# Performance work log

Hardware: AMD Instinct MI355X
Metric: run time of the kernel (lower is better)

The kernel has to match this reference:

```python
import jax, jax.numpy as jnp
import numpy as np

H = 768    # bert hidden size
P = 64     # num dialogue pairs
L = 2 * P  # interleaved (user,system) sequence length
C = 2      # num_classes (CRF tags)
LAM = 0.1  # lambda_mle


def setup_inputs():
    key = jax.random.key(0)
    ks = jax.random.split(key, 21)
    def rn(k, shape, s=0.05):
        return jax.random.normal(k, shape, dtype=jnp.float32) * s
    G = 4 * H
    return {
        "user_repr": rn(ks[0], (P, H), 1.0),
        "system_repr": rn(ks[1], (P, H), 1.0),
        "post_Wih0": rn(ks[2], (2, G, H)), "post_Whh0": rn(ks[3], (2, G, H)), "post_b0": rn(ks[4], (2, G)),
        "post_Wih1": rn(ks[5], (2, G, 2 * H)), "post_Whh1": rn(ks[6], (2, G, H)), "post_b1": rn(ks[7], (2, G)),
        "prior_Wih0": rn(ks[8], (2, G, H)), "prior_Whh0": rn(ks[9], (2, G, H)), "prior_b0": rn(ks[10], (2, G)),
        "prior_Wih1": rn(ks[11], (2, G, 2 * H)), "prior_Whh1": rn(ks[12], (2, G, H)), "prior_b1": rn(ks[13], (2, G)),
        "post_proj_W": rn(ks[14], (C, 2 * H)), "post_proj_b": rn(ks[15], (C,)),
        "prior_proj_W": rn(ks[16], (C, 2 * H)), "prior_proj_b": rn(ks[17], (C,)),
        "transitions": rn(ks[18], (C, C), 0.1),
        "user_I_label": jax.random.randint(ks[19], (1, P), 0, C),
        "system_I_label": jax.random.randint(ks[20], (1, P), 0, C),
    }


def _lstm_dir(x, mask, Wih, Whh, b, reverse):
    # x: [P, L, Din]; mask: [P, L] bool (True = valid step). Masked steps freeze state,
    # so each row computes the LSTM over its own prefix exactly as the per-pair loop does.
    Pn, Ln, _ = x.shape
    Hn = Whh.shape[1]
    xw = jnp.einsum('pld,gd->plg', x, Wih) + b  # [P, L, 4H] input projections (torch gate order i,f,g,o)
    def step(carry, inp):
        h, c = carry
        xw_t, m_t = inp
        gates = xw_t + h @ Whh.T
        i, f, g, o = jnp.split(gates, 4, axis=-1)
        c2 = jax.nn.sigmoid(f) * c + jax.nn.sigmoid(i) * jnp.tanh(g)
        h2 = jax.nn.sigmoid(o) * jnp.tanh(c2)
        m = m_t[:, None]
        h = jnp.where(m, h2, h)
        c = jnp.where(m, c2, c)
        return (h, c), h
    init = (jnp.zeros((Pn, Hn), x.dtype), jnp.zeros((Pn, Hn), x.dtype))
    _, hs = jax.lax.scan(step, init, (jnp.swapaxes(xw, 0, 1), mask.T), reverse=reverse)
    return jnp.swapaxes(hs, 0, 1)  # [P, L, H]


def _bilstm(x, mask, layers):
    for Wih, Whh, b in layers:
        fwd = _lstm_dir(x, mask, Wih[0], Whh[0], b[0], False)
        bwd = _lstm_dir(x, mask, Wih[1], Whh[1], b[1], True)
        x = jnp.concatenate([fwd, bwd], axis=-1)
    return x


def _forward(user_repr, system_repr,
             post_Wih0, post_Whh0, post_b0, post_Wih1, post_Whh1, post_b1,
             prior_Wih0, prior_Whh0, prior_b0, prior_Wih1, prior_Whh1, prior_b1,
             post_proj_W, post_proj_b, prior_proj_W, prior_proj_b, transitions, labs):
    seq = jnp.stack([user_repr, system_repr], axis=1).reshape(L, H)  # interleaved u0,s0,u1,s1,...
    l = 2 * (jnp.arange(P) + 1)                 # prefix length per pair
    t = jnp.arange(L)
    mask = t[None, :] < l[:, None]              # [P, L]
    xb = jnp.broadcast_to(seq[None], (P, L, H))
    # posterior branch: biLSTM over each prefix, then emissions
    post_out = _bilstm(xb, mask, [(post_Wih0, post_Whh0, post_b0), (post_Wih1, post_Whh1, post_b1)])
    em = post_out @ post_proj_W.T + post_proj_b  # [P, L, C]
    mf = mask.astype(em.dtype)
    # CRF gold score per pair
    e_lab = jnp.take_along_axis(em, jnp.broadcast_to(labs[None, :, None], (P, L, 1)), axis=2)[..., 0]
    trans_step = transitions[labs[:-1], labs[1:]]  # [L-1]
    gold = (e_lab * mf).sum(1) + (trans_step[None, :] * mf[:, 1:]).sum(1)
    # CRF forward algorithm (log partition), masked scan over time
    def fstep(alpha, inp):
        em_t, m_t = inp  # [P, C], [P]
        new = jax.nn.logsumexp(alpha[:, :, None] + transitions[None, :, :] + em_t[:, None, :], axis=1)
        return jnp.where(m_t[:, None], new, alpha), None
    alpha, _ = jax.lax.scan(fstep, em[:, 0, :], (jnp.swapaxes(em[:, 1:, :], 0, 1), mask[:, 1:].T))
    total = jax.nn.logsumexp(alpha, axis=1)
    loss_crf = jnp.mean(total - gold)
    # prior branch: prefix minus last token, take last valid hidden
    mask_p = t[None, :] < (l - 1)[:, None]
    prior_out = _bilstm(xb, mask_p, [(prior_Wih0, prior_Whh0, prior_b0), (prior_Wih1, prior_Whh1, prior_b1)])
    prior_last = jnp.take_along_axis(prior_out, jnp.broadcast_to((l - 2)[:, None, None], (P, 1, 2 * H)), axis=1)[:, 0, :]
    prior_emis = prior_last @ prior_proj_W.T + prior_proj_b  # [P, C]
    post_last = jnp.take_along_axis(em, jnp.broadcast_to((l - 1)[:, None, None], (P, 1, C)), axis=1)[:, 0, :]
    loss_mle = jnp.mean((prior_emis - jax.lax.stop_gradient(post_last)) ** 2)
    return loss_crf, loss_mle, loss_crf + LAM * loss_mle


def reference(user_repr, system_repr,
              post_Wih0, post_Whh0, post_b0, post_Wih1, post_Whh1, post_b1,
              prior_Wih0, prior_Whh0, prior_b0, prior_Wih1, prior_Whh1, prior_b1,
              post_proj_W, post_proj_b, prior_proj_W, prior_proj_b, transitions,
              user_I_label, system_I_label):
    labs = jnp.stack([user_I_label[0], system_I_label[0]], axis=1).reshape(L)
    return _forward(user_repr, system_repr,
                    post_Wih0, post_Whh0, post_b0, post_Wih1, post_Whh1, post_b1,
                    prior_Wih0, prior_Whh0, prior_b0, prior_Wih1, prior_Whh1, prior_b1,
                    post_proj_W, post_proj_b, prior_proj_W, prior_proj_b, transitions, labs)
```

## Files before the change

### kernel.cpp

```cpp
#include <hip/hip_runtime.h>


typedef short v8s __attribute__((ext_vector_type(8)));
typedef float v4f __attribute__((ext_vector_type(4)));
typedef unsigned short u16;

#define MFMA(a, b, c) __builtin_amdgcn_mfma_f32_16x16x32_bf16((a), (b), (c), 0, 0, 0)

static constexpr size_t WMAT    = (size_t)96 * 3072 * 8;
static constexpr size_t SLOT16  = (size_t)96 * 16 * 8;
static constexpr size_t SLOT64  = (size_t)96 * 64 * 8;
static constexpr size_t SLOT128 = (size_t)96 * 128 * 8;

static constexpr size_t OFF_EM   = 0;
static constexpr size_t SZ_EM    = (size_t)2 * 64 * 128 * 2 * 4;
static constexpr size_t OFF_XW0  = OFF_EM + SZ_EM;
static constexpr size_t SZ_XW    = (size_t)4 * 128 * 3072 * 4;
static constexpr size_t OFF_XW1  = OFF_XW0 + SZ_XW;
static constexpr size_t OFF_SEQ  = OFF_XW1 + SZ_XW;
static constexpr size_t SZ_SEQ   = SLOT128 * 2;
static constexpr size_t OFF_LABS = OFF_SEQ + SZ_SEQ;
static constexpr size_t OFF_BAR  = OFF_LABS + 512;
static constexpr size_t SZ_BAR   = 16384;
static constexpr size_t OFF_W0   = OFF_BAR + SZ_BAR;
static constexpr size_t SZ_W4    = (size_t)4 * WMAT * 2;
static constexpr size_t OFF_W1X  = OFF_W0 + SZ_W4;
static constexpr size_t OFF_W1R  = OFF_W1X + SZ_W4;
static constexpr size_t OFF_F0   = OFF_W1R + SZ_W4;
static constexpr size_t SZ_F0    = (size_t)2 * 129 * SLOT16 * 2;
static constexpr size_t OFF_H0F  = OFF_F0 + SZ_F0;
static constexpr size_t SZ_H0F   = (size_t)2 * SLOT128 * 2;
static constexpr size_t OFF_B0   = OFF_H0F + SZ_H0F;
static constexpr size_t SZ_S64   = (size_t)2 * 129 * SLOT64 * 2;
static constexpr size_t OFF_F1   = OFF_B0 + SZ_S64;
static constexpr size_t OFF_B1   = OFF_F1 + SZ_S64;
static constexpr size_t WS_NEED  = OFF_B1 + SZ_S64;

static __device__ __forceinline__ u16 f2b(float f) {
  unsigned int u = __float_as_uint(f);
  unsigned int r = (u + 0x7FFFu + ((u >> 16) & 1u)) >> 16;
  return (u16)r;
}
static __device__ __forceinline__ float b2f(u16 u) {
  return __uint_as_float(((unsigned int)u) << 16);
}
static __device__ __forceinline__ float sigf(float x) {
  return 1.0f / (1.0f + __expf(-x));
}
static __device__ __forceinline__ float tanhfast(float x) {
  return 1.0f - 2.0f / (__expf(2.0f * x) + 1.0f);
}
static __device__ __forceinline__ float lse2(float a, float b) {
  float mx = fmaxf(a, b);
  return mx + __logf(__expf(a - mx) + __expf(b - mx));
}

static __device__ __forceinline__ void gl2lds16(const void* g, void* l) {
  __builtin_amdgcn_global_load_lds((const __attribute__((address_space(1))) unsigned int*)g,
                                   (__attribute__((address_space(3))) unsigned int*)l,
                                   16, 0, 0);
}

static __device__ __forceinline__ void tree_bar(unsigned* base, int grp, unsigned target) {
  if (threadIdx.x == 0) {
    asm volatile("s_waitcnt vmcnt(0)" ::: "memory");
    asm volatile("buffer_wbl2 sc1" ::: "memory");
    asm volatile("s_waitcnt vmcnt(0)" ::: "memory");
    unsigned o1 = __hip_atomic_fetch_add(base + grp * 32, 1u,
                                         __ATOMIC_RELAXED, __HIP_MEMORY_SCOPE_AGENT);
    if ((o1 % 6u) == 5u) {
      unsigned o2 = __hip_atomic_fetch_add(base + 256, 1u,
                                           __ATOMIC_RELAXED, __HIP_MEMORY_SCOPE_AGENT);
      if ((o2 % 8u) == 7u) {
        __hip_atomic_fetch_add(base + 288, 1u,
                               __ATOMIC_RELAXED, __HIP_MEMORY_SCOPE_AGENT);
      }
    }
    int guard = 0;
    while (__hip_atomic_load(base + 288, __ATOMIC_RELAXED,
                             __HIP_MEMORY_SCOPE_AGENT) < target) {
      __builtin_amdgcn_s_sleep(4);
      if (++guard > (1 << 20)) break;
    }
    asm volatile("buffer_inv sc0 sc1" ::: "memory");
    asm volatile("s_waitcnt vmcnt(0)" ::: "memory");
  }
  __syncthreads();
}

__global__ void init_zero(u16* f0a, u16* f0b, u16* b0a, u16* b0b,
                          u16* f1a, u16* f1b, u16* b1a, u16* b1b, unsigned* bars) {
  int idx = blockIdx.x * 256 + threadIdx.x;
  if (idx < (int)SLOT16) { f0a[idx] = 0; f0b[idx] = 0; }
  b0a[idx] = 0; b0b[idx] = 0;
  f1a[idx] = 0; f1b[idx] = 0;
  b1a[idx] = 0; b1b[idx] = 0;
  if (idx < 4096) bars[idx] = 0;
}

__global__ void build_seq(const float* user, const float* sysr, const int* ulab,
                          const int* slab, u16* seqkp, int* labs) {
  int idx = blockIdx.x * 256 + threadIdx.x;
  int t = idx / 768;
  int hh = idx - t * 768;
  float v = (t & 1) ? sysr[(t >> 1) * 768 + hh] : user[(t >> 1) * 768 + hh];
  seqkp[((size_t)(hh >> 3) * 128 + t) * 8 + (hh & 7)] = f2b(v);
  if (idx < 128) labs[idx] = (idx & 1) ? slab[idx >> 1] : ulab[idx >> 1];
}

__global__ void cvt_w(const float* postWhh0, const float* priWhh0,
                      const float* postWih1, const float* priWih1,
                      const float* postWhh1, const float* priWhh1,
                      u16* W0kp, u16* W1xkp, u16* W1rkp) {
  int mat = blockIdx.y;
  int grp = mat >> 2;
  int sub = mat & 3;
  int mm = sub >> 1;
  int dirw = sub & 1;
  const float* src;
  int stride, coff;
  u16* dstb;
  if (grp == 0)      { src = mm ? priWhh0 : postWhh0; stride = 768;  coff = 0;   dstb = W0kp; }
  else if (grp == 1) { src = mm ? priWih1 : postWih1; stride = 1536; coff = 768; dstb = W1xkp; }
  else               { src = mm ? priWhh1 : postWhh1; stride = 768;  coff = 0;   dstb = W1rkp; }
  src += (size_t)dirw * 3072 * stride;
  int cid = blockIdx.x * 256 + threadIdx.x;
  int g = cid / 96;
  int kb = cid - g * 96;
  int gate = g / 768;
  int unit = g - gate * 768;
  int gp = unit * 4 + gate;
  const float* s = src + (size_t)g * stride + coff + (size_t)kb * 8;
  union { u16 h[8]; int4 v; } u;
#pragma unroll
  for (int j = 0; j < 8; ++j) u.h[j] = f2b(s[j]);
  ((int4*)(dstb + (size_t)sub * WMAT))[(size_t)kb * 3072 + gp] = u.v;
}

__global__ void __launch_bounds__(256) xw_gemm(const u16* Akp, unsigned long long Astride,
                                               const float* Wm0, const float* Wm1, int wstride,
                                               const float* bm0, const float* bm1, float* out) {
  __shared__ u16 lds[48 * 64 * 8];
  int tid = threadIdx.x;
  int lane = tid & 63;
  int wave = tid >> 6;
  int md = blockIdx.y;
  int m = md >> 1;
  int dir = md & 1;
  const u16* A = Akp + (size_t)m * Astride;
  const float* W = (m ? Wm1 : Wm0) + (size_t)dir * 3072 * wstride;
  const float* b = (m ? bm1 : bm0) + dir * 3072;
  int g0 = blockIdx.x * 64;
  int quad = lane >> 4, l15 = lane & 15;
  v4f acc[2][4];
#pragma unroll
  for (int a = 0; a < 2; ++a)
#pragma unroll
    for (int nt = 0; nt < 4; ++nt) acc[a][nt] = (v4f){0.f, 0.f, 0.f, 0.f};

  for (int hfl = 0; hfl < 2; ++hfl) {
    if (hfl) __syncthreads();
    for (int it = 0; it < 12; ++it) {
      int ck = it * 256 + tid;
      int kb = ck >> 6;
      int r = ck & 63;
      int g = g0 + r;
      const float* s = W + (size_t)g * wstride + (size_t)(hfl * 48 + kb) * 8;
      union { u16 h[8]; int4 v; } u;
#pragma unroll
      for (int j = 0; j < 8; ++j) u.h[j] = f2b(s[j]);
      *(int4*)(lds + (size_t)ck * 8) = u.v;
    }
    __syncthreads();
    for (int lt = 0; lt < 12; ++lt) {
      int kblk = (hfl * 12 + lt) * 4 + quad;
      v8s a0 = ((const v8s*)A)[(size_t)kblk * 128 + (wave * 2 + 0) * 16 + l15];
      v8s a1 = ((const v8s*)A)[(size_t)kblk * 128 + (wave * 2 + 1) * 16 + l15];
#pragma unroll
      for (int nt = 0; nt < 4; ++nt) {
        v8s bb = *(const v8s*)(lds + ((size_t)((lt * 4 + quad) * 64) + nt * 16 + l15) * 8);
        acc[0][nt] = MFMA(a0, bb, acc[0][nt]);
        acc[1][nt] = MFMA(a1, bb, acc[1][nt]);
      }
    }
  }
#pragma unroll
  for (int a = 0; a < 2; ++a)
#pragma unroll
    for (int nt = 0; nt < 4; ++nt) {
      int g = g0 + nt * 16 + l15;
      float bv = b[g];
#pragma unroll
      for (int r = 0; r < 4; ++r) {
        int trow = (wave * 2 + a) * 16 + quad * 4 + r;
        out[(size_t)(md * 128 + trow) * 3072 + g] = acc[a][nt][r] + bv;
      }
    }
}

__global__ void __launch_bounds__(256, 1) phase1_k(const u16* W0kp, const float* xw0,
                                                   u16* B0, u16* F0, u16* h0f,
                                                   unsigned* bars) {
  extern __shared__ u16 ldsraw[];
  v8s* lw = (v8s*)ldsraw;
  const int tid = threadIdx.x;
  const int w = tid >> 6, lane = tid & 63, l15 = lane & 15, l4 = lane >> 4;
  const int b = blockIdx.x;
  const int chain = (b & 7) >> 1;
  const int ci = ((b >> 3) << 1) | (b & 1);
  const int grp = ci / 6;
  const int jb = ci << 4;
  const int m = chain & 1;
  const bool isf = chain >= 2;
  const int mat = m * 2 + (isf ? 0 : 1);
  unsigned* bbase = bars + chain * 512;

  {
    const v8s* Ws = (const v8s*)(W0kp) + (size_t)mat * (WMAT / 8);
    const size_t rowb = (size_t)jb * 4;
    for (int i = 0; i < 24; ++i) {
      int idx = i * 256 + tid;
      int kg = idx >> 6, r = idx & 63;
      gl2lds16(Ws + (size_t)kg * 3072 + rowb + r, (void*)(lw + (i * 256 + (w << 6))));
    }
  }
  __syncthreads();

  const int i0 = w >> 1, j0 = w & 1;
  const int u0 = i0 * 8 + l4, u1 = u0 + 4;
  const int ju0 = jb + u0, ju1 = jb + u1;
  const int p0q = j0 * 32 + l15, p1q = p0q + 16;
  float c00 = 0.f, c01 = 0.f, c10 = 0.f, c11 = 0.f;
  const bool skip = isf && (j0 == 1);
  const bool fep  = isf && (j0 == 0) && (l15 == 0);

  for (int it = 0; it < 128; ++it) {
    const int t = isf ? it : (127 - it);
    const float* xw = xw0 + (size_t)(mat * 128 + t) * 3072;
    float xi0 = xw[ju0], xf0 = xw[768 + ju0], xg0 = xw[1536 + ju0], xo0 = xw[2304 + ju0];
    float xi1 = xw[ju1], xf1 = xw[768 + ju1], xg1 = xw[1536 + ju1], xo1 = xw[2304 + ju1];
    v4f a00 = {0.f, 0.f, 0.f, 0.f}, a01 = a00, a10 = a00, a11 = a00;

    if (isf) {
      if (!skip) {
        const v8s* hs = (const v8s*)(F0 + (size_t)(m * 129 + t) * SLOT16);
#pragma unroll
        for (int kb = 0; kb < 24; ++kb) {
          int kg = kb * 4 + l4;
          v8s A0 = lw[kg * 64 + i0 * 32 + l15];
          v8s A1 = lw[kg * 64 + i0 * 32 + 16 + l15];
          v8s Bb = hs[kg * 16 + l15];
          a00 = MFMA(A0, Bb, a00);
          a10 = MFMA(A1, Bb, a10);
        }
      }
    } else {
      const v8s* hs = (const v8s*)(B0 + (size_t)(m * 129 + t + 1) * SLOT64);
#pragma unroll
      for (int kb = 0; kb < 24; ++kb) {
        int kg = kb * 4 + l4;
        v8s A0 = lw[kg * 64 + i0 * 32 + l15];
        v8s A1 = lw[kg * 64 + i0 * 32 + 16 + l15];
        v8s Bb0 = hs[kg * 64 + p0q];
        v8s Bb1 = hs[kg * 64 + p1q];
        a00 = MFMA(A0, Bb0, a00);
        a01 = MFMA(A0, Bb1, a01);
        a10 = MFMA(A1, Bb0, a10);
        a11 = MFMA(A1, Bb1, a11);
      }
    }

    if (isf) {
      if (fep) {
        float gi = sigf(a00[0] + xi0), gf = sigf(a00[1] + xf0);
        float gg = tanhfast(a00[2] + xg0), go = sigf(a00[3] + xo0);
        float cn = gf * c00 + gi * gg;
        float hn = go * tanhfast(cn);
        c00 = cn;
        u16 hb = f2b(hn);
        F0[(size_t)(m * 129 + t + 1) * SLOT16 + (size_t)(ju0 >> 3) * 16 * 8 + (ju0 & 7)] = hb;
        h0f[(size_t)m * SLOT128 + ((size_t)(ju0 >> 3) * 128 + t) * 8 + (ju0 & 7)] = hb;
        gi = sigf(a10[0] + xi1); gf = sigf(a10[1] + xf1);
        gg = tanhfast(a10[2] + xg1); go = sigf(a10[3] + xo1);
        cn = gf * c10 + gi * gg;
        hn = go * tanhfast(cn);
        c10 = cn;
        hb = f2b(hn);
        F0[(size_t)(m * 129 + t + 1) * SLOT16 + (size_t)(ju1 >> 3) * 16 * 8 + (ju1 & 7)] = hb;
        h0f[(size_t)m * SLOT128 + ((size_t)(ju1 >> 3) * 128 + t) * 8 + (ju1 & 7)] = hb;
      }
    } else {
      u16* hd = B0 + (size_t)(m * 129 + t) * SLOT64;
      auto epi1 = [&](const v4f& ac, float& cc, int ju, int p,
                      float xi, float xf, float xg, float xo) {
        int lenp = 2 * p + 2 - m;
        bool act = t < lenp;
        float gi = sigf(ac[0] + xi), gf = sigf(ac[1] + xf);
        float gg = tanhfast(ac[2] + xg), go = sigf(ac[3] + xo);
        float cn = gf * cc + gi * gg;
        float hn = go * tanhfast(cn);
        cc = act ? cn : 0.f;
        hd[((size_t)(ju >> 3) * 64 + p) * 8 + (ju & 7)] = f2b(act ? hn : 0.f);
      };
      epi1(a00, c00, ju0, p0q, xi0, xf0, xg0, xo0);
      epi1(a01, c01, ju0, p1q, xi0, xf0, xg0, xo0);
      epi1(a10, c10, ju1, p0q, xi1, xf1, xg1, xo1);
      epi1(a11, c11, ju1, p1q, xi1, xf1, xg1, xo1);
    }
    if (it != 127) {
      __syncthreads();
      tree_bar(bbase, grp, (unsigned)(it + 1));
    }
  }
}

__global__ void __launch_bounds__(256, 1) phase2_k(const u16* W1x, const u16* W1r,
                                                   const float* xw1s, const u16* B0,
                                                   u16* F1, u16* B1, unsigned* bars) {
  extern __shared__ u16 ldsraw[];
  v8s* lwr = (v8s*)ldsraw;
  u16* bufb = ldsraw + 49152;
  const int tid = threadIdx.x;
  const int w = tid >> 6, lane = tid & 63, l15 = lane & 15, l4 = lane >> 4;
  const int b = blockIdx.x;
  const int md = (b & 7) >> 1;
  const int ci = ((b >> 3) << 1) | (b & 1);
  const int grp = ci / 6;
  const int jb = ci << 4;
  const int m = md >> 1, dir = md & 1;
  unsigned* bbase = bars + (4 + md) * 512;
  const size_t rowb = (size_t)jb * 4;
  const v8s* Wxs = (const v8s*)(W1x) + (size_t)md * (WMAT / 8);

  {
    const v8s* Wrs = (const v8s*)(W1r) + (size_t)md * (WMAT / 8);
    for (int i = 0; i < 24; ++i) {
      int idx = i * 256 + tid;
      int kg = idx >> 6, r = idx & 63;
      gl2lds16(Wrs + (size_t)kg * 3072 + rowb + r, (void*)(lwr + (i * 256 + (w << 6))));
    }
  }

  const int i0 = w >> 1, j0 = w & 1;
  const int u0 = i0 * 8 + l4, u1 = u0 + 4;
  const int ju0 = jb + u0, ju1 = jb + u1;
  const int p0q = j0 * 32 + l15, p1q = p0q + 16;
  float c00 = 0.f, c01 = 0.f, c10 = 0.f, c11 = 0.f;
  float he00 = 0.f, he01 = 0.f, he10 = 0.f, he11 = 0.f;

  auto stage = [&](int c, int v) {
#pragma unroll
    for (int q = 0; q < 6; ++q) {
      int idx = q * 256 + tid;
      int kgl = idx >> 6, r = idx & 63;
      gl2lds16(Wxs + (size_t)(c * 24 + kgl) * 3072 + rowb + r,
               (void*)(bufb + (size_t)v * 12288 + (size_t)(q * 256 + (w << 6)) * 8));
    }
  };
  stage(0, 0);
  __syncthreads();

  for (int it = 0; it < 128; ++it) {
    const int t = dir ? (127 - it) : it;
    const v8s* hx = (const v8s*)(B0 + (size_t)(m * 129 + t) * SLOT64);
    const v8s* hr = (const v8s*)(dir ? (B1 + (size_t)(m * 129 + t + 1) * SLOT64)
                                     : (F1 + (size_t)(m * 129 + t) * SLOT64));
    const float* xw = xw1s + (size_t)(md * 128 + t) * 3072;
    float xi0 = xw[ju0], xf0 = xw[768 + ju0], xg0 = xw[1536 + ju0], xo0 = xw[2304 + ju0];
    float xi1 = xw[ju1], xf1 = xw[768 + ju1], xg1 = xw[1536 + ju1], xo1 = xw[2304 + ju1];
    v4f a00 = {0.f, 0.f, 0.f, 0.f}, a01 = a00, a10 = a00, a11 = a00;

    auto rpart = [&](int k0) {
#pragma unroll
      for (int k = 0; k < 8; ++k) {
        int kg = (k0 + k) * 4 + l4;
        v8s A0 = lwr[kg * 64 + i0 * 32 + l15];
        v8s A1 = lwr[kg * 64 + i0 * 32 + 16 + l15];
        v8s Bb0 = hr[kg * 64 + p0q];
        v8s Bb1 = hr[kg * 64 + p1q];
        a00 = MFMA(A0, Bb0, a00); a01 = MFMA(A0, Bb1, a01);
        a10 = MFMA(A1, Bb0, a10); a11 = MFMA(A1, Bb1, a11);
      }
    };
    auto xpart = [&](int c, int v) {
      const v8s* bv = (const v8s*)(bufb + (size_t)v * 12288);
#pragma unroll
      for (int k = 0; k < 6; ++k) {
        int kgl = k * 4 + l4;
        int kg = (c * 6 + k) * 4 + l4;
        v8s A0 = bv[kgl * 64 + i0 * 32 + l15];
        v8s A1 = bv[kgl * 64 + i0 * 32 + 16 + l15];
        v8s Bb0 = hx[kg * 64 + p0q];
        v8s Bb1 = hx[kg * 64 + p1q];
        a00 = MFMA(A0, Bb0, a00); a01 = MFMA(A0, Bb1, a01);
        a10 = MFMA(A1, Bb0, a10); a11 = MFMA(A1, Bb1, a11);
      }
    };

    stage(1, 1); rpart(0);  xpart(0, 0); __syncthreads();
    stage(2, 0); rpart(8);  xpart(1, 1); __syncthreads();
    stage(3, 1); rpart(16); xpart(2, 0); __syncthreads();
    xpart(3, 1);

    u16* hd = dir ? (B1 + (size_t)(m * 129 + t) * SLOT64)
                  : (F1 + (size_t)(m * 129 + t + 1) * SLOT64);
    const u16* F1t = (const u16*)(F1 + (size_t)(m * 129 + t) * SLOT64);
    auto epi = [&](const v4f& ac, float& cc, float& he, int ju, int p,
                   float xi, float xf, float xg, float xo) {
      int lenp = 2 * p + 2 - m;
      bool act = t < lenp;
      float gi = sigf(ac[0] + xi), gf = sigf(ac[1] + xf);
      float gg = tanhfast(ac[2] + xg), go = sigf(ac[3] + xo);
      float cn = gf * cc + gi * gg;
      float hn = go * tanhfast(cn);
      float hv;
      if (dir) { hv = act ? hn : 0.f;  cc = act ? cn : 0.f; }
      else     { hv = act ? hn : he;   cc = act ? cn : cc;  }
      he = hv;
      hd[((size_t)(ju >> 3) * 64 + p) * 8 + (ju & 7)] = f2b(hv);
    };
    epi(a00, c00, he00, ju0, p0q, xi0, xf0, xg0, xo0);
    epi(a01, c01, he01, ju0, p1q, xi0, xf0, xg0, xo0);
    epi(a10, c10, he10, ju1, p0q, xi1, xf1, xg1, xo1);
    epi(a11, c11, he11, ju1, p1q, xi1, xf1, xg1, xo1);
    (void)F1t;

    if (it != 127) {
      __syncthreads();
      stage(0, 0);
      tree_bar(bbase, grp, (unsigned)(it + 1));
    }
  }
}

__global__ void __launch_bounds__(256) em_k(const u16* F1, const u16* B1,
                                            const float* pW0, const float* pb0,
                                            const float* pW1, const float* pb1, float* em) {
  int wid = blockIdx.x * 4 + (threadIdx.x >> 6);
  int lane = threadIdx.x & 63;
  int m = wid >> 13;
  int rem = wid & 8191;
  int p = rem >> 7;
  int t = rem & 127;
  const u16* hf = F1 + (size_t)(m * 129 + t + 1) * SLOT64;
  const u16* hb = B1 + (size_t)(m * 129 + t) * SLOT64;
  const float* Pw = m ? pW1 : pW0;
  const float* Pb = m ? pb1 : pb0;
  float s0 = 0.f, s1 = 0.f;
#pragma unroll
  for (int i = 0; i < 12; ++i) {
    int j = i * 64 + lane;
    size_t o = ((size_t)(j >> 3) * 64 + p) * 8 + (j & 7);
    float vf = b2f(hf[o]);
    float vb = b2f(hb[o]);
    s0 += Pw[j] * vf + Pw[768 + j] * vb;
    s1 += Pw[1536 + j] * vf + Pw[2304 + j] * vb;
  }
  for (int off = 32; off; off >>= 1) {
    s0 += __shfl_down(s0, off, 64);
    s1 += __shfl_down(s1, off, 64);
  }
  if (lane == 0) {
    em[((size_t)(m * 64 + p) * 128 + t) * 2 + 0] = s0 + Pb[0];
    em[((size_t)(m * 64 + p) * 128 + t) * 2 + 1] = s1 + Pb[1];
  }
}

__global__ void final_k(const float* em, const int* labs, const float* T, float* out) {
  int p = threadIdx.x;
  const float* emP = em + (size_t)p * 128 * 2;
  int lp = 2 * p + 2;
  float T00 = T[0], T01 = T[1], T10 = T[2], T11 = T[3];
  int prevlab = labs[0];
  float gold = emP[prevlab];
  for (int t = 1; t < lp; ++t) {
    int lb = labs[t];
    gold += emP[t * 2 + lb] + (prevlab ? (lb ? T11 : T10) : (lb ? T01 : T00));
    prevlab = lb;
  }
  float a0 = emP[0], a1 = emP[1];
  for (int t = 1; t < lp; ++t) {
    float n0 = lse2(a0 + T00, a1 + T10) + emP[t * 2];
    float n1 = lse2(a0 + T01, a1 + T11) + emP[t * 2 + 1];
    a0 = n0;
    a1 = n1;
  }
  float crf = lse2(a0, a1) - gold;
  const float* emR = em + (size_t)(64 + p) * 128 * 2;
  int lpr = 2 * p + 1;
  float d0 = emR[(lpr - 1) * 2 + 0] - emP[(lp - 1) * 2 + 0];
  float d1 = emR[(lpr - 1) * 2 + 1] - emP[(lp - 1) * 2 + 1];
  float mse = d0 * d0 + d1 * d1;
  for (int off = 32; off; off >>= 1) {
    crf += __shfl_down(crf, off, 64);
    mse += __shfl_down(mse, off, 64);
  }
  if (p == 0) {
    float lc = crf / 64.f;
    float lm = mse / 128.f;
    out[0] = lc;
    out[1] = lm;
    out[2] = lc + 0.1f * lm;
  }
}

extern "C" void kernel_launch(void* const* d_in, const int* in_sizes, int n_in,
                              void* d_out, int out_size, void* d_ws, size_t ws_size,
                              hipStream_t stream) {
  (void)in_sizes; (void)n_in; (void)out_size;
  if (ws_size < WS_NEED) return;

  const float* user     = (const float*)d_in[0];
  const float* sysr     = (const float*)d_in[1];
  const float* postWih0 = (const float*)d_in[2];
  const float* postWhh0 = (const float*)d_in[3];
  const float* postb0   = (const float*)d_in[4];
  const float* postWih1 = (const float*)d_in[5];
  const float* postWhh1 = (const float*)d_in[6];
  const float* postb1   = (const float*)d_in[7];
  const float* priWih0  = (const float*)d_in[8];
  const float* priWhh0  = (const float*)d_in[9];
  const float* prib0    = (const float*)d_in[10];
  const float* priWih1  = (const float*)d_in[11];
  const float* priWhh1  = (const float*)d_in[12];
  const float* prib1    = (const float*)d_in[13];
  const float* postPW   = (const float*)d_in[14];
  const float* postPb   = (const float*)d_in[15];
  const float* priPW    = (const float*)d_in[16];
  const float* priPb    = (const float*)d_in[17];
  const float* trans    = (const float*)d_in[18];
  const int*   ulab     = (const int*)d_in[19];
  const int*   slab     = (const int*)d_in[20];
  float* out = (float*)d_out;

  char* wsb = (char*)d_ws;
  float* em    = (float*)(wsb + OFF_EM);
  float* xw0   = (float*)(wsb + OFF_XW0);
  float* xw1s  = (float*)(wsb + OFF_XW1);
  u16* seqkp   = (u16*)(wsb + OFF_SEQ);
  int* labs    = (int*)(wsb + OFF_LABS);
  unsigned* bars = (unsigned*)(wsb + OFF_BAR);
  u16* W0kp    = (u16*)(wsb + OFF_W0);
  u16* W1xkp   = (u16*)(wsb + OFF_W1X);
  u16* W1rkp   = (u16*)(wsb + OFF_W1R);
  u16* F0      = (u16*)(wsb + OFF_F0);
  u16* h0f     = (u16*)(wsb + OFF_H0F);
  u16* B0      = (u16*)(wsb + OFF_B0);
  u16* F1      = (u16*)(wsb + OFF_F1);
  u16* B1      = (u16*)(wsb + OFF_B1);

  static bool attr_done = false;
  if (!attr_done) {
    (void)hipFuncSetAttribute(reinterpret_cast<const void*>(phase1_k),
                              hipFuncAttributeMaxDynamicSharedMemorySize, 98304);
    (void)hipFuncSetAttribute(reinterpret_cast<const void*>(phase2_k),
                              hipFuncAttributeMaxDynamicSharedMemorySize, 147456);
    attr_done = true;
  }

  init_zero<<<192, 256, 0, stream>>>(
      F0, F0 + (size_t)129 * SLOT16,
      B0 + (size_t)128 * SLOT64, B0 + (size_t)(129 + 128) * SLOT64,
      F1, F1 + (size_t)129 * SLOT64,
      B1 + (size_t)128 * SLOT64, B1 + (size_t)(129 + 128) * SLOT64, bars);

  build_seq<<<384, 256, 0, stream>>>(user, sysr, ulab, slab, seqkp, labs);

  cvt_w<<<dim3(1152, 12), 256, 0, stream>>>(postWhh0, priWhh0, postWih1, priWih1,
                                            postWhh1, priWhh1, W0kp, W1xkp, W1rkp);

  xw_gemm<<<dim3(48, 4), 256, 0, stream>>>(seqkp, 0ULL, postWih0, priWih0, 768,
                                           postb0, prib0, xw0);

  phase1_k<<<192, 256, 98304, stream>>>(W0kp, xw0, B0, F0, h0f, bars);

  xw_gemm<<<dim3(48, 4), 256, 0, stream>>>(h0f, (unsigned long long)SLOT128,
                                           postWih1, priWih1, 1536, postb1, prib1, xw1s);

  phase2_k<<<192, 256, 147456, stream>>>(W1xkp, W1rkp, xw1s, B0, F1, B1, bars);

  em_k<<<4096, 256, 0, stream>>>(F1, B1, postPW, postPb, priPW, priPb, em);

  final_k<<<1, 64, 0, stream>>>(em, labs, trans, out);
}
```

Measured before the change: 4.312 ms.

## Split grid barrier into signal/wait and overlap input GEMM with barrier wait

Splits the tree barrier into a signal after the step's stores and a wait placed just before the recurrent hidden-state reads. In phase 2 the input-projection MFMA work now runs before the wait. Hidden-state stores use system-coherent stores (sc0 sc1) in place of the L2 writeback and invalidate around each barrier, and the spin sleep is shortened. This aims to hide barrier latency and drop cache-maintenance cost. It risks stale reads, since the cache invalidate on the reading side is gone and readers may pick up cached old hidden states.

```diff
diff --git a/kernel.cpp b/kernel.cpp
--- a/kernel.cpp
+++ b/kernel.cpp
@@ -61,10 +61,14 @@
                                    16, 0, 0);
 }
 
-static __device__ __forceinline__ void tree_bar(unsigned* base, int grp, unsigned target) {
+static __device__ __forceinline__ void st2_sys(u16* p, u16 v) {
+  unsigned int vv = v;
+  asm volatile("global_store_short %0, %1, off sc0 sc1"
+               :: "v"(p), "v"(vv) : "memory");
+}
+
+static __device__ __forceinline__ void bar_signal(unsigned* base, int grp) {
   if (threadIdx.x == 0) {
-    asm volatile("s_waitcnt vmcnt(0)" ::: "memory");
-    asm volatile("buffer_wbl2 sc1" ::: "memory");
     asm volatile("s_waitcnt vmcnt(0)" ::: "memory");
     unsigned o1 = __hip_atomic_fetch_add(base + grp * 32, 1u,
                                          __ATOMIC_RELAXED, __HIP_MEMORY_SCOPE_AGENT);
@@ -76,14 +80,16 @@
                                __ATOMIC_RELAXED, __HIP_MEMORY_SCOPE_AGENT);
       }
     }
+  }
+}
+static __device__ __forceinline__ void bar_wait(unsigned* base, unsigned target) {
+  if (threadIdx.x == 0) {
     int guard = 0;
     while (__hip_atomic_load(base + 288, __ATOMIC_RELAXED,
                              __HIP_MEMORY_SCOPE_AGENT) < target) {
-      __builtin_amdgcn_s_sleep(4);
-      if (++guard > (1 << 20)) break;
-    }
-    asm volatile("buffer_inv sc0 sc1" ::: "memory");
-    asm volatile("s_waitcnt vmcnt(0)" ::: "memory");
+      __builtin_amdgcn_s_sleep(1);
+      if (++guard > (1 << 21)) break;
+    }
   }
   __syncthreads();
 }
@@ -241,6 +247,8 @@
     float xi1 = xw[ju1], xf1 = xw[768 + ju1], xg1 = xw[1536 + ju1], xo1 = xw[2304 + ju1];
     v4f a00 = {0.f, 0.f, 0.f, 0.f}, a01 = a00, a10 = a00, a11 = a00;
 
+    if (it) bar_wait(bbase, (unsigned)it);
+
     if (isf) {
       if (!skip) {
         const v8s* hs = (const v8s*)(F0 + (size_t)(m * 129 + t) * SLOT16);
@@ -278,7 +286,7 @@
         float hn = go * tanhfast(cn);
         c00 = cn;
         u16 hb = f2b(hn);
-        F0[(size_t)(m * 129 + t + 1) * SLOT16 + (size_t)(ju0 >> 3) * 16 * 8 + (ju0 & 7)] = hb;
+        st2_sys(F0 + (size_t)(m * 129 + t + 1) * SLOT16 + (size_t)(ju0 >> 3) * 16 * 8 + (ju0 & 7), hb);
         h0f[(size_t)m * SLOT128 + ((size_t)(ju0 >> 3) * 128 + t) * 8 + (ju0 & 7)] = hb;
         gi = sigf(a10[0] + xi1); gf = sigf(a10[1] + xf1);
         gg = tanhfast(a10[2] + xg1); go = sigf(a10[3] + xo1);
@@ -286,7 +294,7 @@
         hn = go * tanhfast(cn);
         c10 = cn;
         hb = f2b(hn);
-        F0[(size_t)(m * 129 + t + 1) * SLOT16 + (size_t)(ju1 >> 3) * 16 * 8 + (ju1 & 7)] = hb;
+        st2_sys(F0 + (size_t)(m * 129 + t + 1) * SLOT16 + (size_t)(ju1 >> 3) * 16 * 8 + (ju1 & 7), hb);
         h0f[(size_t)m * SLOT128 + ((size_t)(ju1 >> 3) * 128 + t) * 8 + (ju1 & 7)] = hb;
       }
     } else {
@@ -300,17 +308,15 @@
         float cn = gf * cc + gi * gg;
         float hn = go * tanhfast(cn);
         cc = act ? cn : 0.f;
-        hd[((size_t)(ju >> 3) * 64 + p) * 8 + (ju & 7)] = f2b(act ? hn : 0.f);
+        st2_sys(hd + ((size_t)(ju >> 3) * 64 + p) * 8 + (ju & 7), f2b(act ? hn : 0.f));
       };
       epi1(a00, c00, ju0, p0q, xi0, xf0, xg0, xo0);
       epi1(a01, c01, ju0, p1q, xi0, xf0, xg0, xo0);
       epi1(a10, c10, ju1, p0q, xi1, xf1, xg1, xo1);
       epi1(a11, c11, ju1, p1q, xi1, xf1, xg1, xo1);
     }
-    if (it != 127) {
-      __syncthreads();
-      tree_bar(bbase, grp, (unsigned)(it + 1));
-    }
+    __syncthreads();
+    if (it != 127) bar_signal(bbase, grp);
   }
 }
 
@@ -397,14 +403,15 @@
       }
     };
 
-    stage(1, 1); rpart(0);  xpart(0, 0); __syncthreads();
-    stage(2, 0); rpart(8);  xpart(1, 1); __syncthreads();
-    stage(3, 1); rpart(16); xpart(2, 0); __syncthreads();
+    stage(1, 1); xpart(0, 0); __syncthreads();
+    stage(2, 0); xpart(1, 1); __syncthreads();
+    stage(3, 1); xpart(2, 0); __syncthreads();
     xpart(3, 1);
+    if (it) bar_wait(bbase, (unsigned)it);
+    rpart(0); rpart(8); rpart(16);
 
     u16* hd = dir ? (B1 + (size_t)(m * 129 + t) * SLOT64)
                   : (F1 + (size_t)(m * 129 + t + 1) * SLOT64);
-    const u16* F1t = (const u16*)(F1 + (size_t)(m * 129 + t) * SLOT64);
     auto epi = [&](const v4f& ac, float& cc, float& he, int ju, int p,
                    float xi, float xf, float xg, float xo) {
       int lenp = 2 * p + 2 - m;
@@ -417,19 +424,16 @@
       if (dir) { hv = act ? hn : 0.f;  cc = act ? cn : 0.f; }
       else     { hv = act ? hn : he;   cc = act ? cn : cc;  }
       he = hv;
-      hd[((size_t)(ju >> 3) * 64 + p) * 8 + (ju & 7)] = f2b(hv);
+      st2_sys(hd + ((size_t)(ju >> 3) * 64 + p) * 8 + (ju & 7), f2b(hv));
     };
     epi(a00, c00, he00, ju0, p0q, xi0, xf0, xg0, xo0);
     epi(a01, c01, he01, ju0, p1q, xi0, xf0, xg0, xo0);
     epi(a10, c10, he10, ju1, p0q, xi1, xf1, xg1, xo1);
     epi(a11, c11, he11, ju1, p1q, xi1, xf1, xg1, xo1);
-    (void)F1t;
-
-    if (it != 127) {
-      __syncthreads();
-      stage(0, 0);
-      tree_bar(bbase, grp, (unsigned)(it + 1));
-    }
+
+    stage(0, 0);
+    __syncthreads();
+    if (it != 127) bar_signal(bbase, grp);
   }
 }
 
```

Result: faster. 3.670 ms (-14.9%).
